# Optimization experiments

Measured on AMD Instinct MI355X. Metric: run time of the kernel, lower is better.

Reference implementation:

```python
import jax, jax.numpy as jnp
import numpy as np


def setup_inputs() -> dict:
    key = jax.random.key(0)
    ks = jax.random.split(key, 8)
    B, C, W = 8, 512, 2048
    Cq = C // 8
    sq = 1.0 / np.sqrt(C)
    return {
        "x": jax.random.normal(ks[0], (B, C, W), dtype=jnp.float32),
        "Wq": jax.random.normal(ks[1], (Cq, C), dtype=jnp.float32) * sq,
        "bq": jax.random.normal(ks[2], (Cq,), dtype=jnp.float32) * 0.01,
        "Wk": jax.random.normal(ks[3], (Cq, C), dtype=jnp.float32) * sq,
        "bk": jax.random.normal(ks[4], (Cq,), dtype=jnp.float32) * 0.01,
        "Wv": jax.random.normal(ks[5], (C, C), dtype=jnp.float32) * sq,
        "bv": jax.random.normal(ks[6], (C,), dtype=jnp.float32) * 0.01,
        "gamma": jax.random.normal(ks[7], (1,), dtype=jnp.float32),
    }


def reference(x, Wq, bq, Wk, bk, Wv, bv, gamma):
    # x: [B, C, W]; 1x1 Conv1d == channel-mixing matmul.
    q = jnp.einsum("qc,bcw->bqw", Wq, x) + bq[None, :, None]   # [B, C/8, W]
    k = jnp.einsum("qc,bcw->bqw", Wk, x) + bk[None, :, None]   # [B, C/8, W]
    v = jnp.einsum("oc,bcw->bow", Wv, x) + bv[None, :, None]   # [B, C, W]
    # energy[b, i, j] = sum_q q[b, q, i] * k[b, q, j]  (query positions i attend over j)
    energy = jnp.einsum("bqi,bqj->bij", q, k)                  # [B, W, W]
    attn = jax.nn.softmax(energy, axis=-1)                     # [B, W, W]
    # out[b, c, i] = sum_j v[b, c, j] * attn[b, i, j]
    out = jnp.einsum("bcj,bij->bci", v, attn)                  # [B, C, W]
    return gamma[0] * out + x
```

## Files before the change

### kernel.cpp

```cpp
#include <hip/hip_runtime.h>

#define B_  8
#define C_  512
#define CQ_ 64
#define W_  2048

typedef __attribute__((ext_vector_type(8))) short  short8;
typedef __attribute__((ext_vector_type(4))) float  f32x4;
typedef unsigned short ushort;

static constexpr size_t OFF_Q  = 0;
static constexpr size_t OFF_K  = OFF_Q  + (size_t)B_ * CQ_ * W_;
static constexpr size_t OFF_VB = OFF_K  + (size_t)B_ * CQ_ * W_;
static constexpr size_t OFF_E  = OFF_VB + (size_t)B_ * C_ * W_ / 2;
static constexpr size_t OFF_M  = OFF_E  + (size_t)B_ * W_ * W_;
static constexpr size_t OFF_S  = OFF_M  + (size_t)B_ * W_;

static __device__ __forceinline__ ushort f2bf(float f) {
    unsigned int u = __builtin_bit_cast(unsigned int, f);
    u += 0x7fffu + ((u >> 16) & 1u);
    return (ushort)(u >> 16);
}

__global__ __launch_bounds__(256) void k_proj(
    const float* __restrict__ x,
    const float* __restrict__ Wq, const float* __restrict__ bq,
    const float* __restrict__ Wk, const float* __restrict__ bk,
    const float* __restrict__ Wv, const float* __restrict__ bv,
    float* __restrict__ qo, float* __restrict__ ko, ushort* __restrict__ vb)
{
    const int b  = blockIdx.z;
    const int rt = blockIdx.y;
    const int w0 = blockIdx.x * 128;

    const float* Wm; const float* bias; int r0;
    if (rt == 0)      { Wm = Wq; bias = bq; r0 = 0; }
    else if (rt == 1) { Wm = Wk; bias = bk; r0 = 0; }
    else              { Wm = Wv; bias = bv; r0 = (rt - 2) * 64; }

    __shared__ __align__(16) float xs[64][132];
    __shared__ __align__(16) float wt[64][68];

    const int t  = threadIdx.x;
    const int tx = t & 15, ty = t >> 4;

    float acc[4][8];
    #pragma unroll
    for (int i = 0; i < 4; ++i)
        #pragma unroll
        for (int j = 0; j < 8; ++j) acc[i][j] = 0.f;

    for (int ct = 0; ct < 8; ++ct) {
        const float* xsrc = x + ((size_t)b * C_ + ct * 64) * W_ + w0;
        #pragma unroll
        for (int m = 0; m < 8; ++m) {
            int fi = m * 256 + t;
            int cc = fi >> 5;
            int wq = fi & 31;
            *reinterpret_cast<float4*>(&xs[cc][wq * 4]) =
                *reinterpret_cast<const float4*>(xsrc + (size_t)cc * W_ + wq * 4);
        }
        const float* wsrc = Wm + (size_t)r0 * C_ + ct * 64;
        #pragma unroll
        for (int m = 0; m < 4; ++m) {
            int fi = m * 256 + t;
            int r  = fi >> 4;
            int cq = fi & 15;
            float4 vv = *reinterpret_cast<const float4*>(wsrc + (size_t)r * C_ + cq * 4);
            wt[cq * 4 + 0][r] = vv.x;
            wt[cq * 4 + 1][r] = vv.y;
            wt[cq * 4 + 2][r] = vv.z;
            wt[cq * 4 + 3][r] = vv.w;
        }
        __syncthreads();
        #pragma unroll 8
        for (int kk = 0; kk < 64; ++kk) {
            float4 w4 = *reinterpret_cast<const float4*>(&wt[kk][ty * 4]);
            float4 xa = *reinterpret_cast<const float4*>(&xs[kk][tx * 4]);
            float4 xb = *reinterpret_cast<const float4*>(&xs[kk][64 + tx * 4]);
            float wr[4] = {w4.x, w4.y, w4.z, w4.w};
            float xv[8] = {xa.x, xa.y, xa.z, xa.w, xb.x, xb.y, xb.z, xb.w};
            #pragma unroll
            for (int i = 0; i < 4; ++i)
                #pragma unroll
                for (int j = 0; j < 8; ++j)
                    acc[i][j] = fmaf(wr[i], xv[j], acc[i][j]);
        }
        __syncthreads();
    }

    if (rt < 2) {
        float* outp = (rt == 0 ? qo : ko) + (size_t)b * CQ_ * W_;
        #pragma unroll
        for (int i = 0; i < 4; ++i) {
            int r = ty * 4 + i;
            float bb = bias[r];
            float* orow = outp + (size_t)r * W_ + w0;
            float4 o0 = make_float4(acc[i][0] + bb, acc[i][1] + bb, acc[i][2] + bb, acc[i][3] + bb);
            float4 o1 = make_float4(acc[i][4] + bb, acc[i][5] + bb, acc[i][6] + bb, acc[i][7] + bb);
            *reinterpret_cast<float4*>(orow + tx * 4) = o0;
            *reinterpret_cast<float4*>(orow + 64 + tx * 4) = o1;
        }
    } else {
        ushort* outp = vb + (size_t)b * C_ * W_;
        #pragma unroll
        for (int i = 0; i < 4; ++i) {
            int r = r0 + ty * 4 + i;
            float bb = bias[r];
            ushort* orow = outp + (size_t)r * W_ + w0;
            ushort p0[4], p1[4];
            #pragma unroll
            for (int j = 0; j < 4; ++j) { p0[j] = f2bf(acc[i][j] + bb); p1[j] = f2bf(acc[i][4 + j] + bb); }
            unsigned long long v0 = (unsigned long long)p0[0] | ((unsigned long long)p0[1] << 16)
                                  | ((unsigned long long)p0[2] << 32) | ((unsigned long long)p0[3] << 48);
            unsigned long long v1 = (unsigned long long)p1[0] | ((unsigned long long)p1[1] << 16)
                                  | ((unsigned long long)p1[2] << 32) | ((unsigned long long)p1[3] << 48);
            *reinterpret_cast<unsigned long long*>(orow + tx * 4) = v0;
            *reinterpret_cast<unsigned long long*>(orow + 64 + tx * 4) = v1;
        }
    }
}

__global__ __launch_bounds__(256) void k_energy(
    const float* __restrict__ q, const float* __restrict__ k, float* __restrict__ E)
{
    const int b  = blockIdx.z;
    const int i0 = blockIdx.y * 128;
    const int j0 = blockIdx.x * 128;

    __shared__ __align__(16) float qs[64][132];
    __shared__ __align__(16) float ks[64][132];

    const int t  = threadIdx.x;
    const int tx = t & 15, ty = t >> 4;

    const float* qsrc = q + (size_t)b * CQ_ * W_ + i0;
    const float* ksrc = k + (size_t)b * CQ_ * W_ + j0;
    #pragma unroll
    for (int m = 0; m < 8; ++m) {
        int fi = m * 256 + t;
        int qq = fi >> 5;
        int iq = fi & 31;
        *reinterpret_cast<float4*>(&qs[qq][iq * 4]) =
            *reinterpret_cast<const float4*>(qsrc + (size_t)qq * W_ + iq * 4);
        *reinterpret_cast<float4*>(&ks[qq][iq * 4]) =
            *reinterpret_cast<const float4*>(ksrc + (size_t)qq * W_ + iq * 4);
    }
    __syncthreads();

    float acc[8][8];
    #pragma unroll
    for (int i = 0; i < 8; ++i)
        #pragma unroll
        for (int j = 0; j < 8; ++j) acc[i][j] = 0.f;

    #pragma unroll 8
    for (int kk = 0; kk < 64; ++kk) {
        float4 qa = *reinterpret_cast<const float4*>(&qs[kk][ty * 4]);
        float4 qb = *reinterpret_cast<const float4*>(&qs[kk][64 + ty * 4]);
        float4 ka = *reinterpret_cast<const float4*>(&ks[kk][tx * 4]);
        float4 kb = *reinterpret_cast<const float4*>(&ks[kk][64 + tx * 4]);
        float qv[8] = {qa.x, qa.y, qa.z, qa.w, qb.x, qb.y, qb.z, qb.w};
        float kv[8] = {ka.x, ka.y, ka.z, ka.w, kb.x, kb.y, kb.z, kb.w};
        #pragma unroll
        for (int i = 0; i < 8; ++i)
            #pragma unroll
            for (int j = 0; j < 8; ++j)
                acc[i][j] = fmaf(qv[i], kv[j], acc[i][j]);
    }

    float* erow0 = E + ((size_t)b * W_ + i0) * W_ + j0;
    #pragma unroll
    for (int ih = 0; ih < 8; ++ih) {
        int ii = ((ih & 4) << 4) + ty * 4 + (ih & 3);
        float* er = erow0 + (size_t)ii * W_;
        float4 o0 = make_float4(acc[ih][0], acc[ih][1], acc[ih][2], acc[ih][3]);
        float4 o1 = make_float4(acc[ih][4], acc[ih][5], acc[ih][6], acc[ih][7]);
        *reinterpret_cast<float4*>(er + tx * 4) = o0;
        *reinterpret_cast<float4*>(er + 64 + tx * 4) = o1;
    }
}

__global__ __launch_bounds__(256) void k_stats(const float* __restrict__ E,
                                               float* __restrict__ mrow,
                                               float* __restrict__ srow)
{
    const int i = blockIdx.x;
    const int b = blockIdx.y;
    const float* row = E + ((size_t)b * W_ + i) * W_;
    const int t = threadIdx.x;

    float v8[8];
    float lm = -3.0e38f;
    #pragma unroll
    for (int m = 0; m < 8; ++m) {
        v8[m] = row[m * 256 + t];
        lm = fmaxf(lm, v8[m]);
    }
    #pragma unroll
    for (int off = 32; off >= 1; off >>= 1)
        lm = fmaxf(lm, __shfl_xor(lm, off));

    __shared__ float red[8];
    const int wv = t >> 6;
    if ((t & 63) == 0) red[wv] = lm;
    __syncthreads();
    const float bm = fmaxf(fmaxf(red[0], red[1]), fmaxf(red[2], red[3]));

    float ls = 0.f;
    #pragma unroll
    for (int m = 0; m < 8; ++m) ls += __expf(v8[m] - bm);
    #pragma unroll
    for (int off = 32; off >= 1; off >>= 1)
        ls += __shfl_xor(ls, off);
    if ((t & 63) == 0) red[4 + wv] = ls;
    __syncthreads();
    if (t == 0) {
        const float bs = red[4] + red[5] + red[6] + red[7];
        mrow[(size_t)b * W_ + i] = bm;
        srow[(size_t)b * W_ + i] = 1.0f / bs;
    }
}

__global__ __launch_bounds__(256) void k_pv(
    const ushort* __restrict__ vb, const float* __restrict__ E,
    const float* __restrict__ mrow, const float* __restrict__ srow,
    const float* __restrict__ x, const float* __restrict__ gamma,
    float* __restrict__ out)
{
    const int b  = blockIdx.z;
    const int c0 = blockIdx.y * 128;
    const int i0 = blockIdx.x * 128;

    __shared__ __align__(16) ushort Vt[128 * 64];
    __shared__ __align__(16) ushort Pt[128 * 64];

    const int t = threadIdx.x, l = t & 63, wid = t >> 6;
    const int wi = wid & 1, wc = wid >> 1;
    const int lr = l & 15, lk = (l >> 4) * 8;

    int srow4[4], scc4[4];
    float mi4[4], si4[4];
    #pragma unroll
    for (int m = 0; m < 4; ++m) {
        int fi = m * 256 + t;
        srow4[m] = fi >> 3;
        scc4[m]  = fi & 7;
        mi4[m] = mrow[(size_t)b * W_ + i0 + srow4[m]];
        si4[m] = srow[(size_t)b * W_ + i0 + srow4[m]];
    }

    int idxA[4][2], idxB[4][2];
    #pragma unroll
    for (int f = 0; f < 4; ++f)
        #pragma unroll
        for (int kc = 0; kc < 2; ++kc) {
            int rowA = wc * 64 + f * 16 + lr;
            int rowB = wi * 64 + f * 16 + lr;
            idxA[f][kc] = ((rowA * 64) + kc * 32 + lk) ^ ((rowA & 7) << 3);
            idxB[f][kc] = ((rowB * 64) + kc * 32 + lk) ^ ((rowB & 7) << 3);
        }

    f32x4 acc[4][4];
    #pragma unroll
    for (int i = 0; i < 4; ++i)
        #pragma unroll
        for (int j = 0; j < 4; ++j) acc[i][j] = (f32x4){0.f, 0.f, 0.f, 0.f};

    const ushort* vbase = vb + ((size_t)b * C_ + c0) * W_;
    const float*  ebase = E + ((size_t)b * W_ + i0) * W_;

    for (int jt = 0; jt < 32; ++jt) {
        const int j0 = jt * 64;
        #pragma unroll
        for (int m = 0; m < 4; ++m) {
            int row = srow4[m], cc = scc4[m];
            short8 v8 = *reinterpret_cast<const short8*>(vbase + (size_t)row * W_ + j0 + cc * 8);
            int idx = ((row * 64) + cc * 8) ^ ((row & 7) << 3);
            *reinterpret_cast<short8*>(&Vt[idx]) = v8;
        }
        #pragma unroll
        for (int m = 0; m < 4; ++m) {
            int row = srow4[m], cc = scc4[m];
            int idx = ((row * 64) + cc * 8) ^ ((row & 7) << 3);
            const float* eb = ebase + (size_t)row * W_ + j0 + cc * 8;
            float4 e0 = *reinterpret_cast<const float4*>(eb);
            float4 e1 = *reinterpret_cast<const float4*>(eb + 4);
            float mi = mi4[m], si = si4[m];
            short8 ps;
            ps[0] = (short)f2bf(__expf(e0.x - mi) * si);
            ps[1] = (short)f2bf(__expf(e0.y - mi) * si);
            ps[2] = (short)f2bf(__expf(e0.z - mi) * si);
            ps[3] = (short)f2bf(__expf(e0.w - mi) * si);
            ps[4] = (short)f2bf(__expf(e1.x - mi) * si);
            ps[5] = (short)f2bf(__expf(e1.y - mi) * si);
            ps[6] = (short)f2bf(__expf(e1.z - mi) * si);
            ps[7] = (short)f2bf(__expf(e1.w - mi) * si);
            *reinterpret_cast<short8*>(&Pt[idx]) = ps;
        }
        __syncthreads();
        #pragma unroll
        for (int kc = 0; kc < 2; ++kc) {
            short8 a[4], p[4];
            #pragma unroll
            for (int f = 0; f < 4; ++f) {
                a[f] = *reinterpret_cast<const short8*>(&Vt[idxA[f][kc]]);
                p[f] = *reinterpret_cast<const short8*>(&Pt[idxB[f][kc]]);
            }
            #pragma unroll
            for (int fc = 0; fc < 4; ++fc)
                #pragma unroll
                for (int fi = 0; fi < 4; ++fi)
                    acc[fc][fi] = __builtin_amdgcn_mfma_f32_16x16x32_bf16(a[fc], p[fi], acc[fc][fi], 0, 0, 0);
        }
        __syncthreads();
    }

    const float g = gamma[0];
    #pragma unroll
    for (int fc = 0; fc < 4; ++fc) {
        int c = c0 + wc * 64 + fc * 16 + (l >> 4) * 4;
        #pragma unroll
        for (int fi = 0; fi < 4; ++fi) {
            int icol = i0 + wi * 64 + fi * 16 + lr;
            #pragma unroll
            for (int r = 0; r < 4; ++r) {
                size_t addr = ((size_t)b * C_ + c + r) * W_ + icol;
                out[addr] = g * acc[fc][fi][r] + x[addr];
            }
        }
    }
}

extern "C" void kernel_launch(void* const* d_in, const int* in_sizes, int n_in,
                              void* d_out, int out_size, void* d_ws, size_t ws_size,
                              hipStream_t stream)
{
    const float* x     = (const float*)d_in[0];
    const float* Wq    = (const float*)d_in[1];
    const float* bq    = (const float*)d_in[2];
    const float* Wk    = (const float*)d_in[3];
    const float* bk    = (const float*)d_in[4];
    const float* Wv    = (const float*)d_in[5];
    const float* bv    = (const float*)d_in[6];
    const float* gamma = (const float*)d_in[7];
    float* out = (float*)d_out;
    float* ws  = (float*)d_ws;

    float*  q    = ws + OFF_Q;
    float*  k    = ws + OFF_K;
    ushort* vbf  = (ushort*)(ws + OFF_VB);
    float*  E    = ws + OFF_E;
    float*  mrow = ws + OFF_M;
    float*  srow = ws + OFF_S;

    hipLaunchKernelGGL(k_proj,   dim3(W_ / 128, 10, B_), dim3(256), 0, stream,
                       x, Wq, bq, Wk, bk, Wv, bv, q, k, vbf);
    hipLaunchKernelGGL(k_energy, dim3(W_ / 128, W_ / 128, B_), dim3(256), 0, stream,
                       q, k, E);
    hipLaunchKernelGGL(k_stats,  dim3(W_, B_, 1), dim3(256), 0, stream,
                       E, mrow, srow);
    hipLaunchKernelGGL(k_pv,     dim3(W_ / 128, C_ / 128, B_), dim3(256), 0, stream,
                       vbf, E, mrow, srow, x, gamma, out);
}
```

Measured before the change: 369.9 us.

## Move QKV projection to bf16 MFMA with split hi/lo precision for Q/K

Replaces the FP32 FMA projection kernel with a bf16 MFMA kernel. x is pre-transposed and split into bf16 hi/lo parts, and the weights are split the same way. Q and K rows use three MFMA passes (hi*hi, lo*hi, hi*lo) to keep near-fp32 accuracy, while V rows use only hi*hi because V is stored as bf16 anyway. This adds two preprocessing kernels, extra workspace traffic reusing the energy buffer, and uncoalesced scalar output stores from the MFMA layout.

```diff
diff --git a/kernel.cpp b/kernel.cpp
--- a/kernel.cpp
+++ b/kernel.cpp
@@ -4,10 +4,12 @@
 #define C_  512
 #define CQ_ 64
 #define W_  2048
+#define NROW 640
 
 typedef __attribute__((ext_vector_type(8))) short  short8;
 typedef __attribute__((ext_vector_type(4))) float  f32x4;
 typedef unsigned short ushort;
+typedef unsigned long long ull;
 
 static constexpr size_t OFF_Q  = 0;
 static constexpr size_t OFF_K  = OFF_Q  + (size_t)B_ * CQ_ * W_;
@@ -15,108 +17,146 @@
 static constexpr size_t OFF_E  = OFF_VB + (size_t)B_ * C_ * W_ / 2;
 static constexpr size_t OFF_M  = OFF_E  + (size_t)B_ * W_ * W_;
 static constexpr size_t OFF_S  = OFF_M  + (size_t)B_ * W_;
+static constexpr size_t OFF_XTH = OFF_E;
+static constexpr size_t OFF_XTL = OFF_XTH + (size_t)B_ * W_ * C_ / 2;
+static constexpr size_t OFF_WH  = OFF_XTL + (size_t)B_ * W_ * C_ / 2;
+static constexpr size_t OFF_WL  = OFF_WH  + (size_t)NROW * C_ / 2;
 
 static __device__ __forceinline__ ushort f2bf(float f) {
     unsigned int u = __builtin_bit_cast(unsigned int, f);
     u += 0x7fffu + ((u >> 16) & 1u);
     return (ushort)(u >> 16);
 }
-
-__global__ __launch_bounds__(256) void k_proj(
-    const float* __restrict__ x,
-    const float* __restrict__ Wq, const float* __restrict__ bq,
-    const float* __restrict__ Wk, const float* __restrict__ bk,
-    const float* __restrict__ Wv, const float* __restrict__ bv,
+static __device__ __forceinline__ float bf2f(ushort h) {
+    unsigned int u = ((unsigned int)h) << 16;
+    return __builtin_bit_cast(float, u);
+}
+static __device__ __forceinline__ ull pack4(const ushort* p) {
+    return (ull)p[0] | ((ull)p[1] << 16) | ((ull)p[2] << 32) | ((ull)p[3] << 48);
+}
+
+__global__ __launch_bounds__(256) void k_wsplit(
+    const float* __restrict__ Wq, const float* __restrict__ Wk,
+    const float* __restrict__ Wv, ushort* __restrict__ wh, ushort* __restrict__ wl)
+{
+    const int idx = (blockIdx.x * 256 + threadIdx.x) * 4;
+    const int row = idx >> 9, col = idx & 511;
+    const float* src;
+    if (row < 64)       src = Wq + (size_t)row * C_ + col;
+    else if (row < 128) src = Wk + (size_t)(row - 64) * C_ + col;
+    else                src = Wv + (size_t)(row - 128) * C_ + col;
+    float4 v = *reinterpret_cast<const float4*>(src);
+    float vv[4] = {v.x, v.y, v.z, v.w};
+    ushort h[4], lo[4];
+    #pragma unroll
+    for (int j = 0; j < 4; ++j) {
+        h[j]  = f2bf(vv[j]);
+        lo[j] = f2bf(vv[j] - bf2f(h[j]));
+    }
+    *reinterpret_cast<ull*>(wh + idx) = pack4(h);
+    *reinterpret_cast<ull*>(wl + idx) = pack4(lo);
+}
+
+__global__ __launch_bounds__(256) void k_xt(
+    const float* __restrict__ x, ushort* __restrict__ xth, ushort* __restrict__ xtl)
+{
+    const int b = blockIdx.z, c0 = blockIdx.y * 64, w0 = blockIdx.x * 64;
+    __shared__ float ts[64][65];
+    const int t = threadIdx.x;
+    #pragma unroll
+    for (int m = 0; m < 4; ++m) {
+        int fi = m * 256 + t;
+        int c = fi >> 4, c4 = fi & 15;
+        float4 v = *reinterpret_cast<const float4*>(x + ((size_t)b * C_ + c0 + c) * W_ + w0 + c4 * 4);
+        ts[c][c4 * 4 + 0] = v.x; ts[c][c4 * 4 + 1] = v.y;
+        ts[c][c4 * 4 + 2] = v.z; ts[c][c4 * 4 + 3] = v.w;
+    }
+    __syncthreads();
+    #pragma unroll
+    for (int m = 0; m < 4; ++m) {
+        int w  = m * 16 + (t >> 4);
+        int cc = (t & 15) * 4;
+        ushort h[4], lo[4];
+        #pragma unroll
+        for (int j = 0; j < 4; ++j) {
+            float v = ts[cc + j][w];
+            h[j]  = f2bf(v);
+            lo[j] = f2bf(v - bf2f(h[j]));
+        }
+        size_t base = ((size_t)b * W_ + w0 + w) * C_ + c0 + cc;
+        *reinterpret_cast<ull*>(xth + base) = pack4(h);
+        *reinterpret_cast<ull*>(xtl + base) = pack4(lo);
+    }
+}
+
+__global__ __launch_bounds__(512) void k_projm(
+    const ushort* __restrict__ wh, const ushort* __restrict__ wl,
+    const ushort* __restrict__ xth, const ushort* __restrict__ xtl,
+    const float* __restrict__ bq, const float* __restrict__ bk,
+    const float* __restrict__ bv,
     float* __restrict__ qo, float* __restrict__ ko, ushort* __restrict__ vb)
 {
-    const int b  = blockIdx.z;
-    const int rt = blockIdx.y;
-    const int w0 = blockIdx.x * 128;
-
-    const float* Wm; const float* bias; int r0;
-    if (rt == 0)      { Wm = Wq; bias = bq; r0 = 0; }
-    else if (rt == 1) { Wm = Wk; bias = bk; r0 = 0; }
-    else              { Wm = Wv; bias = bv; r0 = (rt - 2) * 64; }
-
-    __shared__ __align__(16) float xs[64][132];
-    __shared__ __align__(16) float wt[64][68];
-
-    const int t  = threadIdx.x;
-    const int tx = t & 15, ty = t >> 4;
-
-    float acc[4][8];
-    #pragma unroll
-    for (int i = 0; i < 4; ++i)
-        #pragma unroll
-        for (int j = 0; j < 8; ++j) acc[i][j] = 0.f;
-
-    for (int ct = 0; ct < 8; ++ct) {
-        const float* xsrc = x + ((size_t)b * C_ + ct * 64) * W_ + w0;
-        #pragma unroll
-        for (int m = 0; m < 8; ++m) {
-            int fi = m * 256 + t;
-            int cc = fi >> 5;
-            int wq = fi & 31;
-            *reinterpret_cast<float4*>(&xs[cc][wq * 4]) =
-                *reinterpret_cast<const float4*>(xsrc + (size_t)cc * W_ + wq * 4);
-        }
-        const float* wsrc = Wm + (size_t)r0 * C_ + ct * 64;
-        #pragma unroll
-        for (int m = 0; m < 4; ++m) {
-            int fi = m * 256 + t;
-            int r  = fi >> 4;
-            int cq = fi & 15;
-            float4 vv = *reinterpret_cast<const float4*>(wsrc + (size_t)r * C_ + cq * 4);
-            wt[cq * 4 + 0][r] = vv.x;
-            wt[cq * 4 + 1][r] = vv.y;
-            wt[cq * 4 + 2][r] = vv.z;
-            wt[cq * 4 + 3][r] = vv.w;
-        }
-        __syncthreads();
-        #pragma unroll 8
-        for (int kk = 0; kk < 64; ++kk) {
-            float4 w4 = *reinterpret_cast<const float4*>(&wt[kk][ty * 4]);
-            float4 xa = *reinterpret_cast<const float4*>(&xs[kk][tx * 4]);
-            float4 xb = *reinterpret_cast<const float4*>(&xs[kk][64 + tx * 4]);
-            float wr[4] = {w4.x, w4.y, w4.z, w4.w};
-            float xv[8] = {xa.x, xa.y, xa.z, xa.w, xb.x, xb.y, xb.z, xb.w};
-            #pragma unroll
-            for (int i = 0; i < 4; ++i)
+    const int b = blockIdx.y, w0 = blockIdx.x * 64;
+    const int t = threadIdx.x, l = t & 63, wid = t >> 6;
+    const int lr = l & 15, lkb = (l >> 4) * 8;
+
+    f32x4 acc[5][4];
+    #pragma unroll
+    for (int m = 0; m < 5; ++m)
+        #pragma unroll
+        for (int n = 0; n < 4; ++n) acc[m][n] = (f32x4){0.f, 0.f, 0.f, 0.f};
+
+    const size_t xbase = ((size_t)b * W_ + w0 + lr) * C_ + lkb;
+
+    for (int kc = 0; kc < 16; ++kc) {
+        short8 bhf[4], blf[4];
+        #pragma unroll
+        for (int n = 0; n < 4; ++n) {
+            bhf[n] = *reinterpret_cast<const short8*>(xth + xbase + (size_t)n * 16 * C_ + kc * 32);
+            blf[n] = *reinterpret_cast<const short8*>(xtl + xbase + (size_t)n * 16 * C_ + kc * 32);
+        }
+        #pragma unroll
+        for (int m = 0; m < 5; ++m) {
+            const int arow = (wid + m * 8) * 16 + lr;
+            const size_t abase = (size_t)arow * C_ + kc * 32 + lkb;
+            short8 ah = *reinterpret_cast<const short8*>(wh + abase);
+            #pragma unroll
+            for (int n = 0; n < 4; ++n)
+                acc[m][n] = __builtin_amdgcn_mfma_f32_16x16x32_bf16(ah, bhf[n], acc[m][n], 0, 0, 0);
+            if (m == 0) {
+                short8 al = *reinterpret_cast<const short8*>(wl + abase);
                 #pragma unroll
-                for (int j = 0; j < 8; ++j)
-                    acc[i][j] = fmaf(wr[i], xv[j], acc[i][j]);
-        }
-        __syncthreads();
-    }
-
-    if (rt < 2) {
-        float* outp = (rt == 0 ? qo : ko) + (size_t)b * CQ_ * W_;
-        #pragma unroll
-        for (int i = 0; i < 4; ++i) {
-            int r = ty * 4 + i;
-            float bb = bias[r];
-            float* orow = outp + (size_t)r * W_ + w0;
-            float4 o0 = make_float4(acc[i][0] + bb, acc[i][1] + bb, acc[i][2] + bb, acc[i][3] + bb);
-            float4 o1 = make_float4(acc[i][4] + bb, acc[i][5] + bb, acc[i][6] + bb, acc[i][7] + bb);
-            *reinterpret_cast<float4*>(orow + tx * 4) = o0;
-            *reinterpret_cast<float4*>(orow + 64 + tx * 4) = o1;
-        }
-    } else {
-        ushort* outp = vb + (size_t)b * C_ * W_;
-        #pragma unroll
-        for (int i = 0; i < 4; ++i) {
-            int r = r0 + ty * 4 + i;
-            float bb = bias[r];
-            ushort* orow = outp + (size_t)r * W_ + w0;
-            ushort p0[4], p1[4];
-            #pragma unroll
-            for (int j = 0; j < 4; ++j) { p0[j] = f2bf(acc[i][j] + bb); p1[j] = f2bf(acc[i][4 + j] + bb); }
-            unsigned long long v0 = (unsigned long long)p0[0] | ((unsigned long long)p0[1] << 16)
-                                  | ((unsigned long long)p0[2] << 32) | ((unsigned long long)p0[3] << 48);
-            unsigned long long v1 = (unsigned long long)p1[0] | ((unsigned long long)p1[1] << 16)
-                                  | ((unsigned long long)p1[2] << 32) | ((unsigned long long)p1[3] << 48);
-            *reinterpret_cast<unsigned long long*>(orow + tx * 4) = v0;
-            *reinterpret_cast<unsigned long long*>(orow + 64 + tx * 4) = v1;
+                for (int n = 0; n < 4; ++n) {
+                    acc[m][n] = __builtin_amdgcn_mfma_f32_16x16x32_bf16(al, bhf[n], acc[m][n], 0, 0, 0);
+                    acc[m][n] = __builtin_amdgcn_mfma_f32_16x16x32_bf16(ah, blf[n], acc[m][n], 0, 0, 0);
+                }
+            }
+        }
+    }
+
+    #pragma unroll
+    for (int m = 0; m < 5; ++m) {
+        const int rbase16 = (wid + m * 8) * 16;
+        #pragma unroll
+        for (int n = 0; n < 4; ++n) {
+            const int wcol = w0 + n * 16 + lr;
+            #pragma unroll
+            for (int r = 0; r < 4; ++r) {
+                const int row = rbase16 + (l >> 4) * 4 + r;
+                float val = acc[m][n][r];
+                if (rbase16 < 64) {
+                    val += bq[row];
+                    qo[((size_t)b * CQ_ + row) * W_ + wcol] = val;
+                } else if (rbase16 < 128) {
+                    const int rl = row - 64;
+                    val += bk[rl];
+                    ko[((size_t)b * CQ_ + rl) * W_ + wcol] = val;
+                } else {
+                    const int rl = row - 128;
+                    val += bv[rl];
+                    vb[((size_t)b * C_ + rl) * W_ + wcol] = f2bf(val);
+                }
+            }
         }
     }
 }
@@ -353,9 +393,17 @@
     float*  E    = ws + OFF_E;
     float*  mrow = ws + OFF_M;
     float*  srow = ws + OFF_S;
-
-    hipLaunchKernelGGL(k_proj,   dim3(W_ / 128, 10, B_), dim3(256), 0, stream,
-                       x, Wq, bq, Wk, bk, Wv, bv, q, k, vbf);
+    ushort* xth  = (ushort*)(ws + OFF_XTH);
+    ushort* xtl  = (ushort*)(ws + OFF_XTL);
+    ushort* wh   = (ushort*)(ws + OFF_WH);
+    ushort* wl   = (ushort*)(ws + OFF_WL);
+
+    hipLaunchKernelGGL(k_wsplit, dim3(NROW * C_ / 1024, 1, 1), dim3(256), 0, stream,
+                       Wq, Wk, Wv, wh, wl);
+    hipLaunchKernelGGL(k_xt,     dim3(W_ / 64, C_ / 64, B_), dim3(256), 0, stream,
+                       x, xth, xtl);
+    hipLaunchKernelGGL(k_projm,  dim3(W_ / 64, B_, 1), dim3(512), 0, stream,
+                       wh, wl, xth, xtl, bq, bk, bv, q, k, vbf);
     hipLaunchKernelGGL(k_energy, dim3(W_ / 128, W_ / 128, B_), dim3(256), 0, stream,
                        q, k, E);
     hipLaunchKernelGGL(k_stats,  dim3(W_, B_, 1), dim3(256), 0, stream,
```

Result: faster. 299.3 us (-19.1%).
